# Optimization experiments

Hardware: AMD Instinct MI355X
Metric: run time of the kernel (lower is better)

## Reference

```python
import jax, jax.numpy as jnp
import numpy as np

B, S, D, H = 4, 2048, 1024, 16
DH = D // H  # 64


def setup_inputs() -> dict:
    key = jax.random.key(0)
    ks = jax.random.split(key, 8)
    scale = 1.0 / np.sqrt(D)  # xavier-ish init for square linears
    return {
        "query": jax.random.normal(ks[0], (B, S, D), jnp.float32),
        "key": jax.random.normal(ks[1], (B, S, D), jnp.float32),
        "value": jax.random.normal(ks[2], (B, S, D), jnp.float32),
        "mask": jax.random.randint(ks[3], (B, 1, 1, S), 0, 2).astype(jnp.bool_),
        "Wq": jax.random.normal(ks[4], (D, D), jnp.float32) * scale,
        "Wk": jax.random.normal(ks[5], (D, D), jnp.float32) * scale,
        "Wv": jax.random.normal(ks[6], (D, D), jnp.float32) * scale,
        "Wo": jax.random.normal(ks[7], (D, D), jnp.float32) * scale,
    }


def _split_heads(x):
    # (B, S, D) -> (B, H, S, DH)
    b, s, _ = x.shape
    return x.reshape(b, s, H, DH).transpose(0, 2, 1, 3)


def reference(query, key, value, mask, Wq, Wk, Wv, Wo):
    # Linear projections (torch Linear: x @ W.T, no bias)
    q = _split_heads(query @ Wq.T)   # (B, H, S, DH)
    k = _split_heads(key @ Wk.T)     # (B, H, S, DH)
    v = _split_heads(value @ Wv.T)   # (B, H, S, DH)

    # Scaled dot-product attention: softmax(QK^T / sqrt(d_head)) V
    scores = jnp.einsum("bhqd,bhkd->bhqk", q, k) / np.sqrt(DH).astype(np.float32)
    # masked_fill_(mask, -1e9): True entries are masked out
    scores = jnp.where(mask, jnp.float32(-1e9), scores)
    attn = jax.nn.softmax(scores, axis=-1)
    # dropout: identity at inference (eval mode)
    ctx = jnp.einsum("bhqk,bhkd->bhqd", attn, v)  # (B, H, S, DH)

    # Merge heads and apply output projection
    ctx = ctx.transpose(0, 2, 1, 3).reshape(query.shape[0], -1, H * DH)
    return ctx @ Wo.T
```

## Files before the change

### kernel.cpp

```cpp
#include <hip/hip_runtime.h>


#define BB 4
#define SS 2048
#define DD 1024
#define HH 16
#define DH 64

typedef __bf16 bf16x8 __attribute__((ext_vector_type(8)));
typedef float floatx4 __attribute__((ext_vector_type(4)));
typedef unsigned short ushortx8 __attribute__((ext_vector_type(8)));
typedef unsigned short ushortx4 __attribute__((ext_vector_type(4)));
typedef unsigned short ushort_t;

__device__ __forceinline__ unsigned short f2bf(float f) {
    unsigned u = __builtin_bit_cast(unsigned, f);
    u += 0x7FFFu + ((u >> 16) & 1u);
    return (unsigned short)(u >> 16);
}

__device__ __forceinline__ bf16x8 ldb(const ushort_t* p) {
    return __builtin_bit_cast(bf16x8, *(const ushortx8*)p);
}

__device__ __forceinline__ void dma16(const ushort_t* g, ushort_t* l) {
    __builtin_amdgcn_global_load_lds(
        (const __attribute__((address_space(1))) unsigned int*)g,
        (__attribute__((address_space(3))) unsigned int*)l, 16, 0, 0);
}

__device__ __forceinline__ floatx4 mfma32(bf16x8 a, bf16x8 b, floatx4 c) {
    return __builtin_amdgcn_mfma_f32_16x16x32_bf16(a, b, c, 0, 0, 0);
}

__device__ __forceinline__ floatx4 fzero() {
    floatx4 z = {0.f, 0.f, 0.f, 0.f};
    return z;
}

__global__ void cvt_f32_bf16(const float* __restrict__ in, ushort_t* __restrict__ out, int n) {
    int i = (blockIdx.x * blockDim.x + threadIdx.x) * 4;
    if (i < n) {
        float4 f = *(const float4*)&in[i];
        ushortx4 o;
        o[0] = f2bf(f.x); o[1] = f2bf(f.y); o[2] = f2bf(f.z); o[3] = f2bf(f.w);
        *(ushortx4*)&out[i] = o;
    }
}

__device__ __forceinline__ void gemm_core(
    const ushort_t* __restrict__ Ab, const ushort_t* __restrict__ Bb,
    floatx4 acc[4][4], ushort_t (*As)[32], ushort_t (*Bs)[32], int tid)
{
    const int wv = tid >> 6, lane = tid & 63;
    const int quad = lane >> 4, lid = lane & 15;
    const int wm = wv & 1, wn = wv >> 1;
    const int r0 = lane >> 2, c0 = (lane & 3) * 8;

#pragma unroll
    for (int i = 0; i < 4; ++i)
#pragma unroll
        for (int j = 0; j < 4; ++j) acc[i][j] = fzero();

    for (int k0 = 0; k0 < DD; k0 += 32) {
        __syncthreads();
#pragma unroll
        for (int s = 0; s < 2; ++s) {
            int seg = wv * 2 + s;
            dma16(&Ab[(size_t)(seg * 16 + r0) * DD + k0 + c0], &As[seg * 16][0]);
            dma16(&Bb[(size_t)(seg * 16 + r0) * DD + k0 + c0], &Bs[seg * 16][0]);
        }
        __syncthreads();

        bf16x8 af[4], bfr[4];
#pragma unroll
        for (int mt = 0; mt < 4; ++mt) af[mt] = ldb(&As[wm * 64 + mt * 16 + lid][quad * 8]);
#pragma unroll
        for (int nt = 0; nt < 4; ++nt) bfr[nt] = ldb(&Bs[wn * 64 + nt * 16 + lid][quad * 8]);
#pragma unroll
        for (int mt = 0; mt < 4; ++mt)
#pragma unroll
            for (int nt = 0; nt < 4; ++nt)
                acc[mt][nt] = mfma32(af[mt], bfr[nt], acc[mt][nt]);
    }
}

__global__ __launch_bounds__(256) void gemm_qkv(
    const ushort_t* __restrict__ Qa, const ushort_t* __restrict__ Ka,
    const ushort_t* __restrict__ Va, const ushort_t* __restrict__ Wqkv,
    const int* __restrict__ maskg,
    ushort_t* __restrict__ Qp, ushort_t* __restrict__ Kp, ushort_t* __restrict__ Vtp)
{
    __shared__ ushort_t As[128][32];
    __shared__ ushort_t Bs[128][32];
    __shared__ ushort_t Ts[4][16][72];

    const int tid = threadIdx.x;
    const int which = blockIdx.x >> 3;
    const int m0 = blockIdx.y * 128;
    const int n0 = blockIdx.x * 128;
    const ushort_t* Ab = (which == 0 ? Qa : which == 1 ? Ka : Va) + (size_t)m0 * DD;
    const ushort_t* Bb = Wqkv + (size_t)n0 * DD;

    floatx4 acc[4][4];
    gemm_core(Ab, Bb, acc, As, Bs, tid);

    const int wv = tid >> 6, lane = tid & 63;
    const int quad = lane >> 4, lid = lane & 15;
    const int wm = wv & 1, wn = wv >> 1;
    const int b = m0 >> 11;
    const int sbase = (m0 & 2047) + wm * 64;
    const int nl0 = n0 - which * 1024 + wn * 64;
    const int sl = lane >> 2, cl = (lane & 3) * 16;

    if (which == 2) {
        const int* maskb = maskg + b * SS;
#pragma unroll
        for (int nt = 0; nt < 4; ++nt) {
#pragma unroll
            for (int mt = 0; mt < 4; ++mt) {
                int sp = sbase + mt * 16 + quad * 4;
                int4 mv = *(const int4*)&maskb[sp];
                ushortx4 o;
                o[0] = mv.x ? (ushort_t)0 : f2bf(acc[mt][nt][0]);
                o[1] = mv.y ? (ushort_t)0 : f2bf(acc[mt][nt][1]);
                o[2] = mv.z ? (ushort_t)0 : f2bf(acc[mt][nt][2]);
                o[3] = mv.w ? (ushort_t)0 : f2bf(acc[mt][nt][3]);
                *(ushortx4*)&Ts[wv][lid][mt * 16 + quad * 4] = o;
            }
            ushortx8 w0 = *(const ushortx8*)&Ts[wv][sl][cl];
            ushortx8 w1 = *(const ushortx8*)&Ts[wv][sl][cl + 8];
            int nl = nl0 + nt * 16 + sl;
            int h = nl >> 6, dh = nl & 63;
            size_t base = (((size_t)b * HH + h) * DH + dh) * SS + sbase + cl;
            *(ushortx8*)&Vtp[base] = w0;
            *(ushortx8*)&Vtp[base + 8] = w1;
        }
    } else {
        ushort_t* P = which ? Kp : Qp;
        const float scl = which ? 1.0f : 0.125f * 1.4426950408889634f;
        const int h = nl0 >> 6;
#pragma unroll
        for (int mt = 0; mt < 4; ++mt) {
#pragma unroll
            for (int nt = 0; nt < 4; ++nt)
#pragma unroll
                for (int r = 0; r < 4; ++r)
                    Ts[wv][quad * 4 + r][nt * 16 + lid] = f2bf(acc[mt][nt][r] * scl);
            ushortx8 w0 = *(const ushortx8*)&Ts[wv][sl][cl];
            ushortx8 w1 = *(const ushortx8*)&Ts[wv][sl][cl + 8];
            int s = sbase + mt * 16 + sl;
            size_t base = (((size_t)b * HH + h) * SS + s) * DH + (nl0 & 63) + cl;
            *(ushortx8*)&P[base] = w0;
            *(ushortx8*)&P[base + 8] = w1;
        }
    }
}

__global__ __launch_bounds__(256) void gemm_o(
    const ushort_t* __restrict__ Cx, const ushort_t* __restrict__ Wo,
    float* __restrict__ Out)
{
    __shared__ ushort_t As[128][32];
    __shared__ ushort_t Bs[128][32];
    const int tid = threadIdx.x;
    const int m0 = blockIdx.y * 128;
    const int n0 = blockIdx.x * 128;

    floatx4 acc[4][4];
    gemm_core(Cx + (size_t)m0 * DD, Wo + (size_t)n0 * DD, acc, As, Bs, tid);

    const int wv = tid >> 6, lane = tid & 63;
    const int quad = lane >> 4, lid = lane & 15;
    const int wm = wv & 1, wn = wv >> 1;
#pragma unroll
    for (int mt = 0; mt < 4; ++mt)
#pragma unroll
        for (int nt = 0; nt < 4; ++nt)
#pragma unroll
            for (int r = 0; r < 4; ++r) {
                int m = m0 + wm * 64 + mt * 16 + quad * 4 + r;
                int n = n0 + wn * 64 + nt * 16 + lid;
                Out[(size_t)m * DD + n] = acc[mt][nt][r];
            }
}

__global__ __launch_bounds__(256) void attn_kernel(
    const ushort_t* __restrict__ Qg, const ushort_t* __restrict__ Kg,
    const ushort_t* __restrict__ Vtg, const int* __restrict__ maskg,
    ushort_t* __restrict__ Ctx)
{
    __shared__ ushort_t Ks[64 * 64];
    __shared__ ushort_t Vts[64 * 64];
    __shared__ ushort_t fmb[SS];

    const int flat = blockIdx.x;
    const int xcd = flat & 7;
    const int slot = flat >> 3;
    const int bh = xcd * 8 + (slot >> 5);
    const int qc = slot & 31;
    const int b = bh >> 4, h = bh & 15;
    const int tid = threadIdx.x;
    const int wv = tid >> 6, lane = tid & 63;
    const int quad = lane >> 4, lid = lane & 15;

    const ushort_t* Qb = Qg + (size_t)bh * SS * DH;
    const ushort_t* Kb = Kg + (size_t)bh * SS * DH;
    const ushort_t* Vtb = Vtg + (size_t)bh * DH * SS;
    const int* maskb = maskg + b * SS;

    {
        const int k8 = tid * 8;
        int4 ma = *(const int4*)&maskb[k8];
        int4 mb2 = *(const int4*)&maskb[k8 + 4];
        ushortx8 f;
        f[0] = ma.x ? (ushort_t)0 : (ushort_t)0x3F80;
        f[1] = ma.y ? (ushort_t)0 : (ushort_t)0x3F80;
        f[2] = ma.z ? (ushort_t)0 : (ushort_t)0x3F80;
        f[3] = ma.w ? (ushort_t)0 : (ushort_t)0x3F80;
        f[4] = mb2.x ? (ushort_t)0 : (ushort_t)0x3F80;
        f[5] = mb2.y ? (ushort_t)0 : (ushort_t)0x3F80;
        f[6] = mb2.z ? (ushort_t)0 : (ushort_t)0x3F80;
        f[7] = mb2.w ? (ushort_t)0 : (ushort_t)0x3F80;
        *(ushortx8*)&fmb[k8] = f;
    }

    const int q0 = qc * 64 + wv * 16;

    bf16x8 qf0, qf1;
    {
        const int row = q0 + lid;
        qf0 = ldb(&Qb[(size_t)row * DH + quad * 8]);
        qf1 = ldb(&Qb[(size_t)row * DH + 32 + quad * 8]);
    }

    int offK[2], offV[2];
#pragma unroll
    for (int s = 0; s < 2; ++s) {
        int idx = wv * 128 + s * 64 + lane;
        int row = idx >> 3;
        int c16 = idx & 7;
        int p = (row & 35) | ((row & 12) << 1) | ((row & 16) >> 2);
        int colu = (c16 ^ (row & 7)) << 3;
        offK[s] = p * DH + colu;
        offV[s] = row * SS + colu;
    }

    floatx4 Oacc[4];
    floatx4 Osum = fzero();
#pragma unroll
    for (int i = 0; i < 4; ++i) Oacc[i] = fzero();

    const ushort_t* Kc = Kb;
    const ushort_t* Vc = Vtb;
    const int swz = (lid & 7) << 3;

    for (int kc = 0; kc < SS / 64; ++kc) {
        __syncthreads();
        dma16(Kc + offK[0], &Ks[(wv * 2 + 0) * 512]);
        dma16(Kc + offK[1], &Ks[(wv * 2 + 1) * 512]);
        dma16(Vc + offV[0], &Vts[(wv * 2 + 0) * 512]);
        dma16(Vc + offV[1], &Vts[(wv * 2 + 1) * 512]);
        __syncthreads();

        floatx4 st[4];
#pragma unroll
        for (int mt = 0; mt < 4; ++mt) {
            const int rb = (mt * 16 + lid) * 64;
            bf16x8 kf0 = ldb(&Ks[rb + ((quad * 8) ^ swz)]);
            bf16x8 kf1 = ldb(&Ks[rb + ((32 + quad * 8) ^ swz)]);
            st[mt] = mfma32(kf1, qf1, mfma32(kf0, qf0, fzero()));
        }

#pragma unroll
        for (int kk = 0; kk < 2; ++kk) {
            bf16x8 pa;
#pragma unroll
            for (int r = 0; r < 4; ++r) {
                pa[r]     = (__bf16)__builtin_amdgcn_exp2f(st[2 * kk][r]);
                pa[r + 4] = (__bf16)__builtin_amdgcn_exp2f(st[2 * kk + 1][r]);
            }
            bf16x8 fm = ldb(&fmb[kc * 64 + kk * 32 + quad * 8]);
            Osum = mfma32(pa, fm, Osum);
#pragma unroll
            for (int nt = 0; nt < 4; ++nt) {
                bf16x8 vb = ldb(&Vts[(nt * 16 + lid) * 64 + ((kk * 32 + quad * 8) ^ swz)]);
                Oacc[nt] = mfma32(pa, vb, Oacc[nt]);
            }
        }

        Kc += 64 * DH;
        Vc += 64;
    }

    float inv[4];
#pragma unroll
    for (int r = 0; r < 4; ++r) inv[r] = 1.0f / Osum[r];

#pragma unroll
    for (int nt = 0; nt < 4; ++nt) {
#pragma unroll
        for (int r = 0; r < 4; ++r) {
            int s = q0 + quad * 4 + r;
            int dh = nt * 16 + lid;
            Ctx[(((size_t)b * SS + s) * HH + h) * DH + dh] = f2bf(Oacc[nt][r] * inv[r]);
        }
    }
}

extern "C" void kernel_launch(void* const* d_in, const int* in_sizes, int n_in,
                              void* d_out, int out_size, void* d_ws, size_t ws_size,
                              hipStream_t stream) {
    const float* q  = (const float*)d_in[0];
    const float* k  = (const float*)d_in[1];
    const float* v  = (const float*)d_in[2];
    const int*   mask = (const int*)d_in[3];
    const float* Wq = (const float*)d_in[4];
    const float* Wk = (const float*)d_in[5];
    const float* Wv = (const float*)d_in[6];
    const float* Wo = (const float*)d_in[7];
    float* out = (float*)d_out;

    char* ws = (char*)d_ws;
    const size_t MB = 1024 * 1024;
    ushort_t* Qin  = (ushort_t*)(ws + 0 * MB);
    ushort_t* Kin  = (ushort_t*)(ws + 16 * MB);
    ushort_t* Vin  = (ushort_t*)(ws + 32 * MB);
    ushort_t* Qp   = (ushort_t*)(ws + 48 * MB);
    ushort_t* Kp   = (ushort_t*)(ws + 64 * MB);
    ushort_t* Vtp  = (ushort_t*)(ws + 80 * MB);
    ushort_t* Wqkv = (ushort_t*)(ws + 96 * MB);
    ushort_t* Wob  = (ushort_t*)(ws + 102 * MB);
    ushort_t* Cx   = Qin;

    const int INEL = BB * SS * DD;
    const int WN = DD * DD;
    cvt_f32_bf16<<<INEL / 1024, 256, 0, stream>>>(q, Qin, INEL);
    cvt_f32_bf16<<<INEL / 1024, 256, 0, stream>>>(k, Kin, INEL);
    cvt_f32_bf16<<<INEL / 1024, 256, 0, stream>>>(v, Vin, INEL);
    cvt_f32_bf16<<<WN / 1024, 256, 0, stream>>>(Wq, Wqkv, WN);
    cvt_f32_bf16<<<WN / 1024, 256, 0, stream>>>(Wk, Wqkv + WN, WN);
    cvt_f32_bf16<<<WN / 1024, 256, 0, stream>>>(Wv, Wqkv + 2 * WN, WN);
    cvt_f32_bf16<<<WN / 1024, 256, 0, stream>>>(Wo, Wob, WN);

    gemm_qkv<<<dim3(24, 64), 256, 0, stream>>>(Qin, Kin, Vin, Wqkv, mask, Qp, Kp, Vtp);
    attn_kernel<<<dim3(2048), 256, 0, stream>>>(Qp, Kp, Vtp, mask, Cx);
    gemm_o<<<dim3(8, 64), 256, 0, stream>>>(Cx, Wob, out);
}
```

Baseline: 384.2 us.

## Double-buffer LDS in GEMMs and attention, remap blocks per XCD, batch conversion launches

The GEMM core and the attention loop now double-buffer their LDS tiles: the next K-slice or KV-chunk is prefetched with global_load_lds while the current one feeds MFMA, and one barrier per iteration replaces two. Both GEMM grids are flattened and remapped so consecutive blocks on the same XCD handle neighbouring tiles, for better L2 reuse. The seven conversion launches are merged into two. The cost is twice the LDS per block, which may reduce occupancy, and the prefetch relies on a single barrier correctly ordering the DMA against reads of the other buffer.

After: 344.5 us. 10.3% less time.

```diff
diff --git a/kernel.cpp b/kernel.cpp
--- a/kernel.cpp
+++ b/kernel.cpp
@@ -38,19 +38,37 @@
     return z;
 }
 
-__global__ void cvt_f32_bf16(const float* __restrict__ in, ushort_t* __restrict__ out, int n) {
+__device__ __forceinline__ void cvt_body(const float* __restrict__ in,
+                                         ushort_t* __restrict__ out) {
     int i = (blockIdx.x * blockDim.x + threadIdx.x) * 4;
-    if (i < n) {
-        float4 f = *(const float4*)&in[i];
-        ushortx4 o;
-        o[0] = f2bf(f.x); o[1] = f2bf(f.y); o[2] = f2bf(f.z); o[3] = f2bf(f.w);
-        *(ushortx4*)&out[i] = o;
-    }
+    float4 f = *(const float4*)&in[i];
+    ushortx4 o;
+    o[0] = f2bf(f.x); o[1] = f2bf(f.y); o[2] = f2bf(f.z); o[3] = f2bf(f.w);
+    *(ushortx4*)&out[i] = o;
+}
+
+__global__ void cvt3(const float* __restrict__ i0, const float* __restrict__ i1,
+                     const float* __restrict__ i2, ushort_t* __restrict__ o0,
+                     ushort_t* __restrict__ o1, ushort_t* __restrict__ o2) {
+    const float* in = blockIdx.y == 0 ? i0 : blockIdx.y == 1 ? i1 : i2;
+    ushort_t* out = blockIdx.y == 0 ? o0 : blockIdx.y == 1 ? o1 : o2;
+    cvt_body(in, out);
+}
+
+__global__ void cvt4(const float* __restrict__ i0, const float* __restrict__ i1,
+                     const float* __restrict__ i2, const float* __restrict__ i3,
+                     ushort_t* __restrict__ o0, ushort_t* __restrict__ o1,
+                     ushort_t* __restrict__ o2, ushort_t* __restrict__ o3) {
+    const float* in = blockIdx.y == 0 ? i0 : blockIdx.y == 1 ? i1
+                     : blockIdx.y == 2 ? i2 : i3;
+    ushort_t* out = blockIdx.y == 0 ? o0 : blockIdx.y == 1 ? o1
+                   : blockIdx.y == 2 ? o2 : o3;
+    cvt_body(in, out);
 }
 
 __device__ __forceinline__ void gemm_core(
     const ushort_t* __restrict__ Ab, const ushort_t* __restrict__ Bb,
-    floatx4 acc[4][4], ushort_t (*As)[32], ushort_t (*Bs)[32], int tid)
+    floatx4 acc[4][4], ushort_t (*As)[128][32], ushort_t (*Bs)[128][32], int tid)
 {
     const int wv = tid >> 6, lane = tid & 63;
     const int quad = lane >> 4, lid = lane & 15;
@@ -62,26 +80,37 @@
 #pragma unroll
         for (int j = 0; j < 4; ++j) acc[i][j] = fzero();
 
+#pragma unroll
+    for (int s = 0; s < 2; ++s) {
+        int seg = wv * 2 + s;
+        dma16(&Ab[(size_t)(seg * 16 + r0) * DD + c0], &As[0][seg * 16][0]);
+        dma16(&Bb[(size_t)(seg * 16 + r0) * DD + c0], &Bs[0][seg * 16][0]);
+    }
+    __syncthreads();
+
+    int cur = 0;
     for (int k0 = 0; k0 < DD; k0 += 32) {
-        __syncthreads();
-#pragma unroll
-        for (int s = 0; s < 2; ++s) {
-            int seg = wv * 2 + s;
-            dma16(&Ab[(size_t)(seg * 16 + r0) * DD + k0 + c0], &As[seg * 16][0]);
-            dma16(&Bb[(size_t)(seg * 16 + r0) * DD + k0 + c0], &Bs[seg * 16][0]);
-        }
-        __syncthreads();
-
+        int nxt = cur ^ 1;
+        if (k0 + 32 < DD) {
+#pragma unroll
+            for (int s = 0; s < 2; ++s) {
+                int seg = wv * 2 + s;
+                dma16(&Ab[(size_t)(seg * 16 + r0) * DD + k0 + 32 + c0], &As[nxt][seg * 16][0]);
+                dma16(&Bb[(size_t)(seg * 16 + r0) * DD + k0 + 32 + c0], &Bs[nxt][seg * 16][0]);
+            }
+        }
         bf16x8 af[4], bfr[4];
 #pragma unroll
-        for (int mt = 0; mt < 4; ++mt) af[mt] = ldb(&As[wm * 64 + mt * 16 + lid][quad * 8]);
-#pragma unroll
-        for (int nt = 0; nt < 4; ++nt) bfr[nt] = ldb(&Bs[wn * 64 + nt * 16 + lid][quad * 8]);
+        for (int mt = 0; mt < 4; ++mt) af[mt] = ldb(&As[cur][wm * 64 + mt * 16 + lid][quad * 8]);
+#pragma unroll
+        for (int nt = 0; nt < 4; ++nt) bfr[nt] = ldb(&Bs[cur][wn * 64 + nt * 16 + lid][quad * 8]);
 #pragma unroll
         for (int mt = 0; mt < 4; ++mt)
 #pragma unroll
             for (int nt = 0; nt < 4; ++nt)
                 acc[mt][nt] = mfma32(af[mt], bfr[nt], acc[mt][nt]);
+        __syncthreads();
+        cur = nxt;
     }
 }
 
@@ -91,14 +120,18 @@
     const int* __restrict__ maskg,
     ushort_t* __restrict__ Qp, ushort_t* __restrict__ Kp, ushort_t* __restrict__ Vtp)
 {
-    __shared__ ushort_t As[128][32];
-    __shared__ ushort_t Bs[128][32];
+    __shared__ ushort_t As[2][128][32];
+    __shared__ ushort_t Bs[2][128][32];
     __shared__ ushort_t Ts[4][16][72];
 
     const int tid = threadIdx.x;
-    const int which = blockIdx.x >> 3;
-    const int m0 = blockIdx.y * 128;
-    const int n0 = blockIdx.x * 128;
+    const int f = blockIdx.x;
+    const int logical = (f & 7) * 192 + (f >> 3);
+    const int by = logical / 24;
+    const int bxx = logical % 24;
+    const int which = bxx >> 3;
+    const int m0 = by * 128;
+    const int n0 = bxx * 128;
     const ushort_t* Ab = (which == 0 ? Qa : which == 1 ? Ka : Va) + (size_t)m0 * DD;
     const ushort_t* Bb = Wqkv + (size_t)n0 * DD;
 
@@ -161,11 +194,14 @@
     const ushort_t* __restrict__ Cx, const ushort_t* __restrict__ Wo,
     float* __restrict__ Out)
 {
-    __shared__ ushort_t As[128][32];
-    __shared__ ushort_t Bs[128][32];
+    __shared__ ushort_t As[2][128][32];
+    __shared__ ushort_t Bs[2][128][32];
     const int tid = threadIdx.x;
-    const int m0 = blockIdx.y * 128;
-    const int n0 = blockIdx.x * 128;
+    const int f = blockIdx.x;
+    const int logical = (f & 7) * 64 + (f >> 3);
+    const int by = logical >> 3, bx = logical & 7;
+    const int m0 = by * 128;
+    const int n0 = bx * 128;
 
     floatx4 acc[4][4];
     gemm_core(Cx + (size_t)m0 * DD, Wo + (size_t)n0 * DD, acc, As, Bs, tid);
@@ -190,8 +226,8 @@
     const ushort_t* __restrict__ Vtg, const int* __restrict__ maskg,
     ushort_t* __restrict__ Ctx)
 {
-    __shared__ ushort_t Ks[64 * 64];
-    __shared__ ushort_t Vts[64 * 64];
+    __shared__ ushort_t Ks[2][64 * 64];
+    __shared__ ushort_t Vts[2][64 * 64];
     __shared__ ushort_t fmb[SS];
 
     const int flat = blockIdx.x;
@@ -213,16 +249,16 @@
         const int k8 = tid * 8;
         int4 ma = *(const int4*)&maskb[k8];
         int4 mb2 = *(const int4*)&maskb[k8 + 4];
-        ushortx8 f;
-        f[0] = ma.x ? (ushort_t)0 : (ushort_t)0x3F80;
-        f[1] = ma.y ? (ushort_t)0 : (ushort_t)0x3F80;
-        f[2] = ma.z ? (ushort_t)0 : (ushort_t)0x3F80;
-        f[3] = ma.w ? (ushort_t)0 : (ushort_t)0x3F80;
-        f[4] = mb2.x ? (ushort_t)0 : (ushort_t)0x3F80;
-        f[5] = mb2.y ? (ushort_t)0 : (ushort_t)0x3F80;
-        f[6] = mb2.z ? (ushort_t)0 : (ushort_t)0x3F80;
-        f[7] = mb2.w ? (ushort_t)0 : (ushort_t)0x3F80;
-        *(ushortx8*)&fmb[k8] = f;
+        ushortx8 fv;
+        fv[0] = ma.x ? (ushort_t)0 : (ushort_t)0x3F80;
+        fv[1] = ma.y ? (ushort_t)0 : (ushort_t)0x3F80;
+        fv[2] = ma.z ? (ushort_t)0 : (ushort_t)0x3F80;
+        fv[3] = ma.w ? (ushort_t)0 : (ushort_t)0x3F80;
+        fv[4] = mb2.x ? (ushort_t)0 : (ushort_t)0x3F80;
+        fv[5] = mb2.y ? (ushort_t)0 : (ushort_t)0x3F80;
+        fv[6] = mb2.z ? (ushort_t)0 : (ushort_t)0x3F80;
+        fv[7] = mb2.w ? (ushort_t)0 : (ushort_t)0x3F80;
+        *(ushortx8*)&fmb[k8] = fv;
     }
 
     const int q0 = qc * 64 + wv * 16;
@@ -251,24 +287,35 @@
 #pragma unroll
     for (int i = 0; i < 4; ++i) Oacc[i] = fzero();
 
-    const ushort_t* Kc = Kb;
-    const ushort_t* Vc = Vtb;
     const int swz = (lid & 7) << 3;
 
+    dma16(Kb + offK[0], &Ks[0][(wv * 2 + 0) * 512]);
+    dma16(Kb + offK[1], &Ks[0][(wv * 2 + 1) * 512]);
+    dma16(Vtb + offV[0], &Vts[0][(wv * 2 + 0) * 512]);
+    dma16(Vtb + offV[1], &Vts[0][(wv * 2 + 1) * 512]);
+    __syncthreads();
+
+    const ushort_t* Kc = Kb + 64 * DH;
+    const ushort_t* Vc = Vtb + 64;
+    int cur = 0;
+
     for (int kc = 0; kc < SS / 64; ++kc) {
-        __syncthreads();
-        dma16(Kc + offK[0], &Ks[(wv * 2 + 0) * 512]);
-        dma16(Kc + offK[1], &Ks[(wv * 2 + 1) * 512]);
-        dma16(Vc + offV[0], &Vts[(wv * 2 + 0) * 512]);
-        dma16(Vc + offV[1], &Vts[(wv * 2 + 1) * 512]);
-        __syncthreads();
+        int nxt = cur ^ 1;
+        if (kc + 1 < SS / 64) {
+            dma16(Kc + offK[0], &Ks[nxt][(wv * 2 + 0) * 512]);
+            dma16(Kc + offK[1], &Ks[nxt][(wv * 2 + 1) * 512]);
+            dma16(Vc + offV[0], &Vts[nxt][(wv * 2 + 0) * 512]);
+            dma16(Vc + offV[1], &Vts[nxt][(wv * 2 + 1) * 512]);
+            Kc += 64 * DH;
+            Vc += 64;
+        }
 
         floatx4 st[4];
 #pragma unroll
         for (int mt = 0; mt < 4; ++mt) {
             const int rb = (mt * 16 + lid) * 64;
-            bf16x8 kf0 = ldb(&Ks[rb + ((quad * 8) ^ swz)]);
-            bf16x8 kf1 = ldb(&Ks[rb + ((32 + quad * 8) ^ swz)]);
+            bf16x8 kf0 = ldb(&Ks[cur][rb + ((quad * 8) ^ swz)]);
+            bf16x8 kf1 = ldb(&Ks[cur][rb + ((32 + quad * 8) ^ swz)]);
             st[mt] = mfma32(kf1, qf1, mfma32(kf0, qf0, fzero()));
         }
 
@@ -284,13 +331,12 @@
             Osum = mfma32(pa, fm, Osum);
 #pragma unroll
             for (int nt = 0; nt < 4; ++nt) {
-                bf16x8 vb = ldb(&Vts[(nt * 16 + lid) * 64 + ((kk * 32 + quad * 8) ^ swz)]);
+                bf16x8 vb = ldb(&Vts[cur][(nt * 16 + lid) * 64 + ((kk * 32 + quad * 8) ^ swz)]);
                 Oacc[nt] = mfma32(pa, vb, Oacc[nt]);
             }
         }
-
-        Kc += 64 * DH;
-        Vc += 64;
+        __syncthreads();
+        cur = nxt;
     }
 
     float inv[4];
@@ -335,15 +381,11 @@
 
     const int INEL = BB * SS * DD;
     const int WN = DD * DD;
-    cvt_f32_bf16<<<INEL / 1024, 256, 0, stream>>>(q, Qin, INEL);
-    cvt_f32_bf16<<<INEL / 1024, 256, 0, stream>>>(k, Kin, INEL);
-    cvt_f32_bf16<<<INEL / 1024, 256, 0, stream>>>(v, Vin, INEL);
-    cvt_f32_bf16<<<WN / 1024, 256, 0, stream>>>(Wq, Wqkv, WN);
-    cvt_f32_bf16<<<WN / 1024, 256, 0, stream>>>(Wk, Wqkv + WN, WN);
-    cvt_f32_bf16<<<WN / 1024, 256, 0, stream>>>(Wv, Wqkv + 2 * WN, WN);
-    cvt_f32_bf16<<<WN / 1024, 256, 0, stream>>>(Wo, Wob, WN);
-
-    gemm_qkv<<<dim3(24, 64), 256, 0, stream>>>(Qin, Kin, Vin, Wqkv, mask, Qp, Kp, Vtp);
+    cvt3<<<dim3(INEL / 1024, 3), 256, 0, stream>>>(q, k, v, Qin, Kin, Vin);
+    cvt4<<<dim3(WN / 1024, 4), 256, 0, stream>>>(Wq, Wk, Wv, Wo,
+                                                 Wqkv, Wqkv + WN, Wqkv + 2 * WN, Wob);
+
+    gemm_qkv<<<dim3(1536), 256, 0, stream>>>(Qin, Kin, Vin, Wqkv, mask, Qp, Kp, Vtp);
     attn_kernel<<<dim3(2048), 256, 0, stream>>>(Qp, Kp, Vtp, mask, Cx);
-    gemm_o<<<dim3(8, 64), 256, 0, stream>>>(Cx, Wob, out);
-}
+    gemm_o<<<dim3(512), 256, 0, stream>>>(Cx, Wob, out);
+}
```
